# Performance work log

Hardware: AMD Instinct MI355X
Metric: run time of the kernel (lower is better)

The kernel has to match this reference:

```python
import jax, jax.numpy as jnp
import numpy as np

B, S, D = 4, 2048, 1024
H, HD = 16, 64
NDIM = 2                      # 2D RoPE (position_ids last dim)
PER_DIM = 2 * (HD // (2 * NDIM))   # 32 rotated dims per spatial axis
HALF = PER_DIM // 2                # 16
EPS = 1e-6


def setup_inputs() -> dict:
    key = jax.random.key(0)
    ks = jax.random.split(key, 10)
    sc = 0.02
    return {
        "hidden_states": jax.random.normal(ks[0], (B, S, D), jnp.float32),
        "cos": jax.random.uniform(ks[1], (B, S, HD), jnp.float32, -1.0, 1.0),
        "sin": jax.random.uniform(ks[2], (B, S, HD), jnp.float32, -1.0, 1.0),
        "position_ids": jax.random.randint(ks[3], (B, S, NDIM), 0, S, jnp.int64 if jax.config.x64_enabled else jnp.int32),
        # torch nn.Linear weights are [out_features, in_features]
        "wq": jax.random.normal(ks[4], (H * HD, D), jnp.float32) * sc,
        "wk": jax.random.normal(ks[5], (H * HD, D), jnp.float32) * sc,
        "wv": jax.random.normal(ks[6], (H * HD, D), jnp.float32) * sc,
        "wo": jax.random.normal(ks[7], (D, H * HD), jnp.float32) * sc,
        "q_scale": jnp.ones((HD,), jnp.float32),
        "k_scale": jnp.ones((HD,), jnp.float32),
    }


def _rms_norm(x, scale=None, eps=EPS):
    n = x * jax.lax.rsqrt(jnp.mean(x * x, axis=-1, keepdims=True) + eps)
    return n * scale if scale is not None else n


def _rotate_half(x):
    x1, x2 = x[..., :HALF], x[..., HALF:]
    return jnp.concatenate([-x2, x1], axis=-1)


def _rope2d(x, cos, sin):
    # x: [B,S,H,HD]; cos/sin: [B,S,HD]; rotate each NDIM chunk independently
    parts = []
    for k in range(NDIM):
        sl = slice(k * PER_DIM, (k + 1) * PER_DIM)
        xp = x[..., sl]
        cp = cos[:, :, None, sl]
        sp = sin[:, :, None, sl]
        parts.append(xp * cp + _rotate_half(xp) * sp)
    return jnp.concatenate(parts, axis=-1)


def reference(hidden_states, cos, sin, position_ids, wq, wk, wv, wo, q_scale, k_scale):
    b, s, _ = hidden_states.shape
    # QKV projections (clamp buffers default to +/-inf -> identity)
    q = (hidden_states @ wq.T).reshape(b, s, H, HD)
    k = (hidden_states @ wk.T).reshape(b, s, H, HD)
    v = (hidden_states @ wv.T).reshape(b, s, H, HD)
    # per-head RMSNorm (q/k with scale, v without)
    q = _rms_norm(q, q_scale)
    k = _rms_norm(k, k_scale)
    v = _rms_norm(v)
    # 2D RoPE on q and k
    q = _rope2d(q, cos, sin)
    k = _rope2d(k, cos, sin)
    # SDPA with scale=1.0 (as in the source), heads-major layout
    scores = jnp.einsum('bqhd,bkhd->bhqk', q, k)
    attn = jax.nn.softmax(scores, axis=-1)
    out = jnp.einsum('bhqk,bkhd->bqhd', attn, v).reshape(b, s, H * HD)
    return out @ wo.T
```

## Files before the change

### kernel.cpp

```cpp
#include <hip/hip_runtime.h>
#include <hip/hip_bf16.h>
#include <stdint.h>
#include <stddef.h>

#define B_ 4
#define S_ 2048
#define D_ 1024
#define H_ 16
#define HD_ 64
#define NTOK (B_*S_)
#define HDIM (H_*HD_)
#define LOG2E 1.44269504088896f

typedef __bf16 bf16_t;
typedef __bf16 bf16x4 __attribute__((ext_vector_type(4)));
typedef __bf16 bf16x8 __attribute__((ext_vector_type(8)));
typedef float floatx4 __attribute__((ext_vector_type(4)));

#define MFMA16(a,b,c)  __builtin_amdgcn_mfma_f32_16x16x32_bf16((a),(b),(c),0,0,0)

__device__ __forceinline__ void async_cp16(const bf16_t* g, bf16_t* l) {
    typedef __attribute__((address_space(1))) const unsigned int gu32;
    typedef __attribute__((address_space(3))) unsigned int lu32;
    __builtin_amdgcn_global_load_lds((gu32*)g, (lu32*)l, 16, 0, 0);
}

__device__ __forceinline__ bf16x8 cat44(bf16x4 a, bf16x4 b) {
    union { bf16x4 h[2]; bf16x8 v; } u;
    u.h[0] = a; u.h[1] = b;
    return u.v;
}

struct Cvt6 {
    const float* s[5]; bf16_t* d[5]; int n4[5];
    const float* cs; const float* sn; float* cpk;
};

__global__ __launch_bounds__(256) void cvt6(Cvt6 p) {
    const int z = blockIdx.y;
    if (z < 5) {
        const float4* __restrict__ src = (const float4*)p.s[z];
        bf16x4* __restrict__ dst = (bf16x4*)p.d[z];
        const int n4 = p.n4[z];
        for (int i = blockIdx.x * 256 + threadIdx.x; i < n4; i += gridDim.x * 256) {
            const float4 v = src[i];
            dst[i] = (bf16x4){(bf16_t)v.x, (bf16_t)v.y, (bf16_t)v.z, (bf16_t)v.w};
        }
    } else {
        const int N = B_*S_*HD_;
        for (int i = blockIdx.x * 256 + threadIdx.x; i < N; i += gridDim.x * 256) {
            const int bs = i >> 6, d = i & 63;
            float2 cs2;
            cs2.x = p.cs[i];
            cs2.y = p.sn[i];
            *(float2*)(p.cpk + (size_t)bs*128 + (d & 15)*8 + (d >> 4)*2) = cs2;
        }
    }
}

struct GemmPtrs {
    const bf16_t* A[3]; const bf16_t* W[3]; void* C[3];
    const float* cpk; const float* qs; const float* ks;
};

template<int MODE>
__global__ __launch_bounds__(256, 3) void gemm_nt(GemmPtrs p, int K) {
    __shared__ bf16_t lds[4*4096];
    bf16_t* lA0 = lds;
    bf16_t* lA1 = lds + 4096;
    bf16_t* lB0 = lds + 8192;
    bf16_t* lB1 = lds + 12288;
    const bf16_t* __restrict__ A = p.A[blockIdx.z];
    const bf16_t* __restrict__ W = p.W[blockIdx.z];
    const int lin  = blockIdx.x + 8*blockIdx.y;
    const int slot = lin >> 3;
    const int mblk = (lin & 7)*8 + (slot >> 3);
    const int nblk = slot & 7;
    const int m0 = mblk * 128;
    const int n0 = nblk * 128;
    const int t = threadIdx.x;
    const int lane = t & 63;
    const int wave = t >> 6;
    const int wm = wave >> 1;
    const int wn = wave & 1;
    const int l16 = lane & 15;
    const int quad = lane >> 4;

    const int srow0 = wave*32 + (lane >> 2);
    const int skc   = (lane & 3) * 8;
    const int gsw   = ((srow0 ^ (srow0 >> 2)) & 3) * 8;
    const int glw   = ((l16 ^ (l16 >> 2)) & 3) * 8;

    floatx4 acc[4][4] = {};

    for (int k0 = 0; k0 < K; k0 += 64) {
        #pragma unroll
        for (int c = 0; c < 2; ++c) {
            const int row = srow0 + c*16;
            const size_t ao = (size_t)(m0+row)*K + k0 + (skc ^ gsw);
            const size_t wo = (size_t)(n0+row)*K + k0 + (skc ^ gsw);
            async_cp16(&A[ao],      &lA0[row*32 + skc]);
            async_cp16(&A[ao + 32], &lA1[row*32 + skc]);
            async_cp16(&W[wo],      &lB0[row*32 + skc]);
            async_cp16(&W[wo + 32], &lB1[row*32 + skc]);
        }
        __syncthreads();
        {
            bf16x8 af[4], bfr[4];
            #pragma unroll
            for (int i = 0; i < 4; ++i) {
                af[i]  = *(const bf16x8*)(&lA0[(wm*64 + i*16 + l16)*32 + (quad*8 ^ glw)]);
                bfr[i] = *(const bf16x8*)(&lB0[(wn*64 + i*16 + l16)*32 + (quad*8 ^ glw)]);
            }
            #pragma unroll
            for (int i = 0; i < 4; ++i)
                #pragma unroll
                for (int j = 0; j < 4; ++j)
                    acc[i][j] = MFMA16(af[i], bfr[j], acc[i][j]);
        }
        {
            bf16x8 af[4], bfr[4];
            #pragma unroll
            for (int i = 0; i < 4; ++i) {
                af[i]  = *(const bf16x8*)(&lA1[(wm*64 + i*16 + l16)*32 + (quad*8 ^ glw)]);
                bfr[i] = *(const bf16x8*)(&lB1[(wn*64 + i*16 + l16)*32 + (quad*8 ^ glw)]);
            }
            #pragma unroll
            for (int i = 0; i < 4; ++i)
                #pragma unroll
                for (int j = 0; j < 4; ++j)
                    acc[i][j] = MFMA16(af[i], bfr[j], acc[i][j]);
        }
        __syncthreads();
    }

    if (MODE == 1) {
        const int z = blockIdx.z;
        const int h = nblk*2 + wn;
        float inv[4][4];
        #pragma unroll
        for (int i = 0; i < 4; ++i) {
            #pragma unroll
            for (int r = 0; r < 4; ++r) {
                float ssq = 0.f;
                #pragma unroll
                for (int j = 0; j < 4; ++j) ssq += acc[i][j][r]*acc[i][j][r];
                ssq += __shfl_xor(ssq, 1);
                ssq += __shfl_xor(ssq, 2);
                ssq += __shfl_xor(ssq, 4);
                ssq += __shfl_xor(ssq, 8);
                inv[i][r] = rsqrtf(ssq*(1.f/64.f) + 1e-6f);
            }
        }
        if (z < 2) {
            bf16_t* __restrict__ C = (bf16_t*)p.C[z];
            const float* __restrict__ scp = (z == 0) ? p.qs : p.ks;
            const float scl = (z == 0) ? LOG2E : 1.f;
            float qsl[4];
            #pragma unroll
            for (int j = 0; j < 4; ++j) qsl[j] = scp[j*16 + l16] * scl;
            #pragma unroll
            for (int i = 0; i < 4; ++i) {
                #pragma unroll
                for (int r = 0; r < 4; ++r) {
                    const int m = m0 + wm*64 + i*16 + quad*4 + r;
                    const int b = m >> 11, s = m & (S_-1);
                    float nv[4];
                    #pragma unroll
                    for (int j = 0; j < 4; ++j) nv[j] = acc[i][j][r] * inv[i][r] * qsl[j];
                    const float* cb = p.cpk + ((size_t)b*S_ + s)*128 + l16*8;
                    const float4 L0 = *(const float4*)(cb);
                    const float4 L1 = *(const float4*)(cb + 4);
                    bf16_t* crow = &C[(((size_t)b*H_ + h)*S_ + s)*HD_ + l16];
                    crow[0]  = (bf16_t)(nv[0]*L0.x - nv[1]*L0.y);
                    crow[16] = (bf16_t)(nv[1]*L0.z + nv[0]*L0.w);
                    crow[32] = (bf16_t)(nv[2]*L1.x - nv[3]*L1.y);
                    crow[48] = (bf16_t)(nv[3]*L1.z + nv[2]*L1.w);
                }
            }
        } else {
            bf16_t* __restrict__ Vt = (bf16_t*)p.C[2];
            const int mbase = m0 + wm*64;
            const int b = mbase >> 11;
            const int sbase = mbase & (S_-1);
            bf16_t* wl = lds + wave*2304;
            #pragma unroll
            for (int ps = 0; ps < 2; ++ps) {
                #pragma unroll
                for (int jj = 0; jj < 2; ++jj) {
                    const int j = ps*2 + jj;
                    const int dd = jj*16 + l16;
                    #pragma unroll
                    for (int i = 0; i < 4; ++i) {
                        bf16x4 pk;
                        #pragma unroll
                        for (int r = 0; r < 4; ++r)
                            pk[r] = (bf16_t)(acc[i][j][r] * inv[i][r]);
                        *(bf16x4*)(&wl[dd*72 + i*16 + quad*4]) = pk;
                    }
                }
                const int dloc = lane >> 1;
                const int kh = (lane & 1) * 32;
                bf16_t* dst = &Vt[((size_t)(b*H_ + h)*HD_ + ps*32 + dloc)*S_ + sbase + kh];
                #pragma unroll
                for (int c = 0; c < 4; ++c) {
                    const bf16x8 vv = *(const bf16x8*)(&wl[dloc*72 + kh + c*8]);
                    *(bf16x8*)(&dst[c*8]) = vv;
                }
            }
        }
    } else {
        float* __restrict__ C = (float*)p.C[blockIdx.z];
        #pragma unroll
        for (int i = 0; i < 4; ++i) {
            const int mb = m0 + wm*64 + i*16 + quad*4;
            #pragma unroll
            for (int j = 0; j < 4; ++j) {
                const int n = n0 + wn*64 + j*16 + l16;
                #pragma unroll
                for (int r = 0; r < 4; ++r)
                    C[(size_t)(mb + r)*HDIM + n] = acc[i][j][r];
            }
        }
    }
}

__global__ __launch_bounds__(512, 4) void flash_attn(
    const bf16_t* __restrict__ qn, const bf16_t* __restrict__ kn,
    const bf16_t* __restrict__ vt, bf16_t* __restrict__ attn_out) {
    __shared__ __align__(16) bf16_t sh[16384];

    const int lin  = blockIdx.x + 8*blockIdx.y;
    const int slot = lin >> 3;
    const int bh   = (lin & 7)*8 + (slot >> 3);
    const int q0   = (slot & 7) * 256;
    const int b  = bh >> 4;
    const int h  = bh & 15;
    const int t = threadIdx.x;
    const int wave = t >> 6;
    const int lane = t & 63;
    const int l16 = lane & 15;
    const int quad = lane >> 4;
    const floatx4 finit = {-46.f, -46.f, -46.f, -46.f};

    const bf16_t* Q  = qn + (size_t)bh * S_ * HD_;
    const bf16_t* K  = kn + (size_t)bh * S_ * HD_;
    const bf16_t* Vt = vt + (size_t)bh * HD_ * S_;

    bf16x8 qf[2][2];
    #pragma unroll
    for (int rb = 0; rb < 2; ++rb) {
        const int qrow = q0 + wave*32 + rb*16 + l16;
        qf[rb][0] = *(const bf16x8*)(&Q[(size_t)qrow*HD_ + quad*8]);
        qf[rb][1] = *(const bf16x8*)(&Q[(size_t)qrow*HD_ + 32 + quad*8]);
    }

    floatx4 accO[2][4] = {};
    float accL[2] = {0.f, 0.f};

    const int sgrow = (wave & 3)*16 + l16;
    const int sgcol = (wave >> 2)*32 + quad*8;
    const int kwoff = (wave & 3)*1024 + (wave >> 2)*512 + lane*8;
    const int vU    = ((wave & 3)*2 + (wave >> 2))*64 + ((2*quad) & 3)*16 + l16;
    const int vwoff = vU*8 + (quad >> 1)*4;

    async_cp16(&K[(size_t)sgrow*HD_ + sgcol], &sh[kwoff]);
    {
        const bf16x8 v0 = *(const bf16x8*)(&Vt[(size_t)sgrow*S_ + sgcol]);
        union { bf16x8 v; bf16x4 hh[2]; } uv; uv.v = v0;
        *(bf16x4*)(&sh[8192 + vwoff])       = uv.hh[0];
        *(bf16x4*)(&sh[8192 + vwoff + 128]) = uv.hh[1];
    }

    bf16x8 vpre;
    for (int i = 0; i < S_/64; ++i) {
        __syncthreads();
        const bf16_t* lK = sh + (i & 1)*4096;
        const bf16_t* lV = sh + 8192 + (i & 1)*4096;
        const bool more = (i + 1 < S_/64);
        if (more) {
            const int ktn = (i + 1) * 64;
            async_cp16(&K[(size_t)(ktn + sgrow)*HD_ + sgcol],
                       &sh[((i+1) & 1)*4096 + kwoff]);
            vpre = *(const bf16x8*)(&Vt[(size_t)sgrow*S_ + ktn + sgcol]);
        }

        __builtin_amdgcn_s_setprio(1);
        bf16x4 pf[2][4];
        #pragma unroll
        for (int ct = 0; ct < 4; ++ct) {
            const bf16x8 kf0 = *(const bf16x8*)(&lK[ct*1024 + lane*8]);
            const bf16x8 kf1 = *(const bf16x8*)(&lK[ct*1024 + 512 + lane*8]);
            #pragma unroll
            for (int rb = 0; rb < 2; ++rb) {
                floatx4 s = MFMA16(kf0, qf[rb][0], finit);
                s = MFMA16(kf1, qf[rb][1], s);
                const float e0 = __builtin_amdgcn_exp2f(s[0]);
                const float e1 = __builtin_amdgcn_exp2f(s[1]);
                const float e2 = __builtin_amdgcn_exp2f(s[2]);
                const float e3 = __builtin_amdgcn_exp2f(s[3]);
                accL[rb] += (e0 + e1) + (e2 + e3);
                bf16x4 pb;
                pb[0] = (bf16_t)e0; pb[1] = (bf16_t)e1;
                pb[2] = (bf16_t)e2; pb[3] = (bf16_t)e3;
                pf[rb][ct] = pb;
            }
        }
        bf16x8 pb8[2][2];
        #pragma unroll
        for (int rb = 0; rb < 2; ++rb) {
            pb8[rb][0] = cat44(pf[rb][0], pf[rb][1]);
            pb8[rb][1] = cat44(pf[rb][2], pf[rb][3]);
        }
        #pragma unroll
        for (int dt = 0; dt < 4; ++dt) {
            #pragma unroll
            for (int c = 0; c < 2; ++c) {
                const bf16x8 vf = *(const bf16x8*)(&lV[(dt*2 + c)*512 + lane*8]);
                accO[0][dt] = MFMA16(vf, pb8[0][c], accO[0][dt]);
                accO[1][dt] = MFMA16(vf, pb8[1][c], accO[1][dt]);
            }
        }
        __builtin_amdgcn_s_setprio(0);

        if (more) {
            bf16_t* nV = sh + 8192 + ((i+1) & 1)*4096;
            union { bf16x8 v; bf16x4 hh[2]; } uv; uv.v = vpre;
            *(bf16x4*)(&nV[vwoff])       = uv.hh[0];
            *(bf16x4*)(&nV[vwoff + 128]) = uv.hh[1];
        }
    }

    __syncthreads();
    bf16_t* W = sh + wave * (16*72);
    #pragma unroll
    for (int rb = 0; rb < 2; ++rb) {
        float lr = accL[rb];
        lr += __shfl_xor(lr, 16);
        lr += __shfl_xor(lr, 32);
        const float inv = 1.f / lr;
        #pragma unroll
        for (int dt = 0; dt < 4; ++dt)
            #pragma unroll
            for (int r = 0; r < 4; ++r)
                W[l16*72 + dt*16 + quad*4 + r] = (bf16_t)(accO[rb][dt][r] * inv);
        #pragma unroll
        for (int half = 0; half < 2; ++half) {
            const int qr = half*8 + (lane >> 3);
            const bf16x8 o = *(const bf16x8*)(&W[qr*72 + (lane & 7)*8]);
            const int srw = q0 + wave*32 + rb*16 + qr;
            *(bf16x8*)(&attn_out[((size_t)b*S_ + srw)*HDIM + h*HD_ + (lane & 7)*8]) = o;
        }
    }
}

extern "C" void kernel_launch(void* const* d_in, const int* in_sizes, int n_in,
                              void* d_out, int out_size, void* d_ws, size_t ws_size,
                              hipStream_t stream) {
    (void)in_sizes; (void)n_in; (void)out_size; (void)ws_size;
    const float* X  = (const float*)d_in[0];
    const float* cs = (const float*)d_in[1];
    const float* sn = (const float*)d_in[2];
    const float* wq = (const float*)d_in[4];
    const float* wk = (const float*)d_in[5];
    const float* wv = (const float*)d_in[6];
    const float* wo = (const float*)d_in[7];
    const float* qs = (const float*)d_in[8];
    const float* ks = (const float*)d_in[9];
    float* out = (float*)d_out;

    const size_t PROJ = (size_t)NTOK * HDIM;
    const size_t WSZ  = (size_t)HDIM * D_;
    bf16_t* ws   = (bf16_t*)d_ws;
    bf16_t* Xb   = ws;
    bf16_t* wqb  = ws + PROJ;
    bf16_t* wkb  = wqb + WSZ;
    bf16_t* wvb  = wkb + WSZ;
    bf16_t* wob  = wvb + WSZ;
    bf16_t* qb   = wob + WSZ;
    bf16_t* kb   = qb + PROJ;
    bf16_t* vb   = kb + PROJ;
    bf16_t* vt   = vb;
    bf16_t* attn = Xb;
    float*  cpk  = out;

    Cvt6 cp;
    cp.s[0] = X;  cp.d[0] = Xb;  cp.n4[0] = (int)(PROJ/4);
    cp.s[1] = wq; cp.d[1] = wqb; cp.n4[1] = (int)(WSZ/4);
    cp.s[2] = wk; cp.d[2] = wkb; cp.n4[2] = (int)(WSZ/4);
    cp.s[3] = wv; cp.d[3] = wvb; cp.n4[3] = (int)(WSZ/4);
    cp.s[4] = wo; cp.d[4] = wob; cp.n4[4] = (int)(WSZ/4);
    cp.cs = cs; cp.sn = sn; cp.cpk = cpk;
    cvt6<<<dim3(1024, 6), 256, 0, stream>>>(cp);

    GemmPtrs g1;
    g1.A[0] = Xb;  g1.A[1] = Xb;  g1.A[2] = Xb;
    g1.W[0] = wqb; g1.W[1] = wkb; g1.W[2] = wvb;
    g1.C[0] = qb;  g1.C[1] = kb;  g1.C[2] = vt;
    g1.cpk = cpk; g1.qs = qs; g1.ks = ks;
    gemm_nt<1><<<dim3(HDIM/128, NTOK/128, 3), 256, 0, stream>>>(g1, D_);

    flash_attn<<<dim3(S_/256, B_*H_), 512, 0, stream>>>(qb, kb, vt, attn);

    GemmPtrs g2;
    g2.A[0] = attn; g2.W[0] = wob; g2.C[0] = out;
    g2.A[1] = attn; g2.W[1] = wob; g2.C[1] = out;
    g2.A[2] = attn; g2.W[2] = wob; g2.C[2] = out;
    g2.cpk = cpk; g2.qs = qs; g2.ks = ks;
    gemm_nt<2><<<dim3(HDIM/128, NTOK/128, 1), 256, 0, stream>>>(g2, HDIM);
}
```

Baseline: 258.2 us.

## Double-buffer GEMM K-loop with prefetch of next 32-wide K tile

Restructures the GEMM main loop from a load-then-compute step of 64 K columns into a ping-pong over two LDS buffers of 32 K columns each. The next tile's async global-to-LDS copies are issued before computing on the current one, so memory latency can overlap with MFMA work, and there is now one barrier per iteration. The XOR swizzle on LDS addresses is dropped, which risks bank conflicts on the fragment reads. An extra barrier is added before the epilogue, which reuses LDS.

```diff
diff --git a/kernel.cpp b/kernel.cpp
--- a/kernel.cpp
+++ b/kernel.cpp
@@ -66,10 +66,6 @@
 template<int MODE>
 __global__ __launch_bounds__(256, 3) void gemm_nt(GemmPtrs p, int K) {
     __shared__ bf16_t lds[4*4096];
-    bf16_t* lA0 = lds;
-    bf16_t* lA1 = lds + 4096;
-    bf16_t* lB0 = lds + 8192;
-    bf16_t* lB1 = lds + 12288;
     const bf16_t* __restrict__ A = p.A[blockIdx.z];
     const bf16_t* __restrict__ W = p.W[blockIdx.z];
     const int lin  = blockIdx.x + 8*blockIdx.y;
@@ -88,50 +84,45 @@
 
     const int srow0 = wave*32 + (lane >> 2);
     const int skc   = (lane & 3) * 8;
-    const int gsw   = ((srow0 ^ (srow0 >> 2)) & 3) * 8;
-    const int glw   = ((l16 ^ (l16 >> 2)) & 3) * 8;
+    const size_t aoff = (size_t)(m0+srow0)*K + skc;
+    const size_t woff = (size_t)(n0+srow0)*K + skc;
+    const int l0 = srow0*32 + skc;
 
     floatx4 acc[4][4] = {};
 
-    for (int k0 = 0; k0 < K; k0 += 64) {
-        #pragma unroll
-        for (int c = 0; c < 2; ++c) {
-            const int row = srow0 + c*16;
-            const size_t ao = (size_t)(m0+row)*K + k0 + (skc ^ gsw);
-            const size_t wo = (size_t)(n0+row)*K + k0 + (skc ^ gsw);
-            async_cp16(&A[ao],      &lA0[row*32 + skc]);
-            async_cp16(&A[ao + 32], &lA1[row*32 + skc]);
-            async_cp16(&W[wo],      &lB0[row*32 + skc]);
-            async_cp16(&W[wo + 32], &lB1[row*32 + skc]);
-        }
+    #pragma unroll
+    for (int c = 0; c < 2; ++c) {
+        async_cp16(&A[aoff + (size_t)c*16*K], &lds[l0 + c*512]);
+        async_cp16(&W[woff + (size_t)c*16*K], &lds[8192 + l0 + c*512]);
+    }
+
+    const int NT = K >> 5;
+    for (int tt = 0; tt < NT; ++tt) {
         __syncthreads();
-        {
-            bf16x8 af[4], bfr[4];
-            #pragma unroll
-            for (int i = 0; i < 4; ++i) {
-                af[i]  = *(const bf16x8*)(&lA0[(wm*64 + i*16 + l16)*32 + (quad*8 ^ glw)]);
-                bfr[i] = *(const bf16x8*)(&lB0[(wn*64 + i*16 + l16)*32 + (quad*8 ^ glw)]);
-            }
-            #pragma unroll
-            for (int i = 0; i < 4; ++i)
-                #pragma unroll
-                for (int j = 0; j < 4; ++j)
-                    acc[i][j] = MFMA16(af[i], bfr[j], acc[i][j]);
-        }
-        {
-            bf16x8 af[4], bfr[4];
-            #pragma unroll
-            for (int i = 0; i < 4; ++i) {
-                af[i]  = *(const bf16x8*)(&lA1[(wm*64 + i*16 + l16)*32 + (quad*8 ^ glw)]);
-                bfr[i] = *(const bf16x8*)(&lB1[(wn*64 + i*16 + l16)*32 + (quad*8 ^ glw)]);
-            }
-            #pragma unroll
-            for (int i = 0; i < 4; ++i)
-                #pragma unroll
-                for (int j = 0; j < 4; ++j)
-                    acc[i][j] = MFMA16(af[i], bfr[j], acc[i][j]);
-        }
-        __syncthreads();
+        const int cur = tt & 1;
+        bf16_t* la = lds + cur*4096;
+        bf16_t* lb = lds + 8192 + cur*4096;
+        if (tt + 1 < NT) {
+            const int ks = (tt + 1) << 5;
+            bf16_t* na = lds + (cur^1)*4096;
+            bf16_t* nb = lds + 8192 + (cur^1)*4096;
+            #pragma unroll
+            for (int c = 0; c < 2; ++c) {
+                async_cp16(&A[aoff + ks + (size_t)c*16*K], &na[l0 + c*512]);
+                async_cp16(&W[woff + ks + (size_t)c*16*K], &nb[l0 + c*512]);
+            }
+        }
+        bf16x8 af[4], bfr[4];
+        #pragma unroll
+        for (int i = 0; i < 4; ++i) {
+            af[i]  = *(const bf16x8*)(&la[(wm*64 + i*16 + l16)*32 + quad*8]);
+            bfr[i] = *(const bf16x8*)(&lb[(wn*64 + i*16 + l16)*32 + quad*8]);
+        }
+        #pragma unroll
+        for (int i = 0; i < 4; ++i)
+            #pragma unroll
+            for (int j = 0; j < 4; ++j)
+                acc[i][j] = MFMA16(af[i], bfr[j], acc[i][j]);
     }
 
     if (MODE == 1) {
@@ -179,6 +170,7 @@
                 }
             }
         } else {
+            __syncthreads();
             bf16_t* __restrict__ Vt = (bf16_t*)p.C[2];
             const int mbase = m0 + wm*64;
             const int b = mbase >> 11;
```

After: 275.1 us. +6.6%, slower.

## Load K and V fragments directly from global memory in flash attention

Applied to the files above, without the earlier changes.

Removes the double-buffered LDS staging of K and V tiles (async copy plus register-staged V writes and per-iteration barriers) and has each wave read its MFMA operands straight from global memory. This eliminates block-wide synchronisation and shrinks shared memory to the epilogue buffer, which could raise occupancy. In exchange, all eight waves redundantly fetch the same K/V data through the cache hierarchy, and loads are no longer prefetched ahead of use, exposing global latency.

```diff
diff --git a/kernel.cpp b/kernel.cpp
--- a/kernel.cpp
+++ b/kernel.cpp
@@ -228,7 +228,7 @@
 __global__ __launch_bounds__(512, 4) void flash_attn(
     const bf16_t* __restrict__ qn, const bf16_t* __restrict__ kn,
     const bf16_t* __restrict__ vt, bf16_t* __restrict__ attn_out) {
-    __shared__ __align__(16) bf16_t sh[16384];
+    __shared__ __align__(16) bf16_t sh[8*16*72];
 
     const int lin  = blockIdx.x + 8*blockIdx.y;
     const int slot = lin >> 3;
@@ -258,39 +258,16 @@
     floatx4 accO[2][4] = {};
     float accL[2] = {0.f, 0.f};
 
-    const int sgrow = (wave & 3)*16 + l16;
-    const int sgcol = (wave >> 2)*32 + quad*8;
-    const int kwoff = (wave & 3)*1024 + (wave >> 2)*512 + lane*8;
-    const int vU    = ((wave & 3)*2 + (wave >> 2))*64 + ((2*quad) & 3)*16 + l16;
-    const int vwoff = vU*8 + (quad >> 1)*4;
-
-    async_cp16(&K[(size_t)sgrow*HD_ + sgcol], &sh[kwoff]);
-    {
-        const bf16x8 v0 = *(const bf16x8*)(&Vt[(size_t)sgrow*S_ + sgcol]);
-        union { bf16x8 v; bf16x4 hh[2]; } uv; uv.v = v0;
-        *(bf16x4*)(&sh[8192 + vwoff])       = uv.hh[0];
-        *(bf16x4*)(&sh[8192 + vwoff + 128]) = uv.hh[1];
-    }
-
-    bf16x8 vpre;
     for (int i = 0; i < S_/64; ++i) {
-        __syncthreads();
-        const bf16_t* lK = sh + (i & 1)*4096;
-        const bf16_t* lV = sh + 8192 + (i & 1)*4096;
-        const bool more = (i + 1 < S_/64);
-        if (more) {
-            const int ktn = (i + 1) * 64;
-            async_cp16(&K[(size_t)(ktn + sgrow)*HD_ + sgcol],
-                       &sh[((i+1) & 1)*4096 + kwoff]);
-            vpre = *(const bf16x8*)(&Vt[(size_t)sgrow*S_ + ktn + sgcol]);
-        }
+        const int kt = i * 64;
 
         __builtin_amdgcn_s_setprio(1);
         bf16x4 pf[2][4];
         #pragma unroll
         for (int ct = 0; ct < 4; ++ct) {
-            const bf16x8 kf0 = *(const bf16x8*)(&lK[ct*1024 + lane*8]);
-            const bf16x8 kf1 = *(const bf16x8*)(&lK[ct*1024 + 512 + lane*8]);
+            const bf16_t* krow = &K[(size_t)(kt + ct*16 + l16)*HD_ + quad*8];
+            const bf16x8 kf0 = *(const bf16x8*)(krow);
+            const bf16x8 kf1 = *(const bf16x8*)(krow + 32);
             #pragma unroll
             for (int rb = 0; rb < 2; ++rb) {
                 floatx4 s = MFMA16(kf0, qf[rb][0], finit);
@@ -314,24 +291,18 @@
         }
         #pragma unroll
         for (int dt = 0; dt < 4; ++dt) {
+            const bf16_t* vrow = &Vt[(size_t)(dt*16 + l16)*S_ + kt + quad*4];
             #pragma unroll
             for (int c = 0; c < 2; ++c) {
-                const bf16x8 vf = *(const bf16x8*)(&lV[(dt*2 + c)*512 + lane*8]);
+                const bf16x8 vf = cat44(*(const bf16x4*)(vrow + c*32),
+                                        *(const bf16x4*)(vrow + c*32 + 16));
                 accO[0][dt] = MFMA16(vf, pb8[0][c], accO[0][dt]);
                 accO[1][dt] = MFMA16(vf, pb8[1][c], accO[1][dt]);
             }
         }
         __builtin_amdgcn_s_setprio(0);
-
-        if (more) {
-            bf16_t* nV = sh + 8192 + ((i+1) & 1)*4096;
-            union { bf16x8 v; bf16x4 hh[2]; } uv; uv.v = vpre;
-            *(bf16x4*)(&nV[vwoff])       = uv.hh[0];
-            *(bf16x4*)(&nV[vwoff + 128]) = uv.hh[1];
-        }
-    }
-
-    __syncthreads();
+    }
+
     bf16_t* W = sh + wave * (16*72);
     #pragma unroll
     for (int rb = 0; rb < 2; ++rb) {
```

Result: slower. 532.6 us (+106.3%).
